# Kernel tuning notes

Measured on AMD Instinct MI355X. Metric: run time of the kernel, lower is better.

The kernel has to match this reference:

```python
import jax, jax.numpy as jnp
import numpy as np

N_II = 100000      # item nodes
N_UIU = 200000     # user + item nodes
D = 64             # embedding_dim
E_II = 600000
E_UIU = 1200000
L_II = 3           # num_layers_ii
L_UIU = 3          # num_layers_uiu
N_USERS = 100000   # items occupy indices [N_USERS, N_USERS+N_II)


def _lightgcn_embedding(x, edge_index, edge_weight, num_layers, num_nodes):
    """PyG LightGCN.get_embedding: symmetric gcn_norm (no self loops) + mean over layer outputs."""
    src, dst = edge_index[0], edge_index[1]
    # gcn_norm: deg over target nodes, weighted by edge_weight
    deg = jax.ops.segment_sum(edge_weight, dst, num_segments=num_nodes)
    deg_inv_sqrt = jnp.where(deg > 0, jax.lax.rsqrt(jnp.where(deg > 0, deg, 1.0)), 0.0)
    norm = deg_inv_sqrt[src] * edge_weight * deg_inv_sqrt[dst]  # [E]
    alpha = 1.0 / (num_layers + 1)
    out = x * alpha
    for _ in range(num_layers):
        # SpMM: gather source embeddings, scale, scatter-add to targets
        x = jax.ops.segment_sum(norm[:, None] * x[src], dst, num_segments=num_nodes)  # [N, D]
        out = out + x * alpha
    return out


def setup_inputs() -> dict:
    key = jax.random.key(0)
    k1, k2, k3, k4, k5, k6 = jax.random.split(key, 6)
    return {
        "emb_ii": jax.random.normal(k1, (N_II, D), dtype=jnp.float32),
        "emb_uiu": jax.random.normal(k2, (N_UIU, D), dtype=jnp.float32),
        "edge_attr_ii": jax.random.uniform(k3, (E_II,), dtype=jnp.float32),
        "edge_attr_uiu": jax.random.uniform(k4, (E_UIU,), dtype=jnp.float32),
        "edge_index_ii": jax.random.randint(k5, (2, E_II), 0, N_II, dtype=jnp.int32),
        "edge_index_uiu": jax.random.randint(k6, (2, E_UIU), 0, N_UIU, dtype=jnp.int32),
        # contiguous item block starting at N_USERS (node_mask_item.nonzero())
        "item_idx": jnp.arange(N_II, dtype=jnp.int32) + N_USERS,
    }


def reference(emb_ii, emb_uiu, edge_attr_ii, edge_attr_uiu,
              edge_index_ii, edge_index_uiu, item_idx):
    # item-item graph propagation
    h_ii = _lightgcn_embedding(emb_ii, edge_index_ii, edge_attr_ii, L_II, N_II)  # [N_II, D]
    # write item embeddings into the user-item embedding table
    emb_uiu = emb_uiu.at[item_idx].set(h_ii)
    # user-item graph propagation
    h_uiu = _lightgcn_embedding(emb_uiu, edge_index_uiu, edge_attr_uiu, L_UIU, N_UIU)  # [N_UIU, D]
    return h_uiu
```

## Files before the change

kernel.cpp:

```cpp
#include <hip/hip_runtime.h>


#define D       64
#define N_II    100000
#define N_UIU   200000
#define E_II    600000
#define E_UIU   1200000
#define N_USERS 100000
#define B       256
#define CR_K    8
#define FE_K    4

__device__ __forceinline__ unsigned short f2bf(float f) {
    unsigned u = __float_as_uint(f);
    u += 0x7fffu + ((u >> 16) & 1u);
    return (unsigned short)(u >> 16);
}
__device__ __forceinline__ void bf8_fma(float acc[8], uint4 p, float v) {
    acc[0] += v * __uint_as_float(p.x << 16);
    acc[1] += v * __uint_as_float(p.x & 0xffff0000u);
    acc[2] += v * __uint_as_float(p.y << 16);
    acc[3] += v * __uint_as_float(p.y & 0xffff0000u);
    acc[4] += v * __uint_as_float(p.z << 16);
    acc[5] += v * __uint_as_float(p.z & 0xffff0000u);
    acc[6] += v * __uint_as_float(p.w << 16);
    acc[7] += v * __uint_as_float(p.w & 0xffff0000u);
}
__device__ __forceinline__ void bf8_add(float acc[8], uint4 p) {
    acc[0] += __uint_as_float(p.x << 16);
    acc[1] += __uint_as_float(p.x & 0xffff0000u);
    acc[2] += __uint_as_float(p.y << 16);
    acc[3] += __uint_as_float(p.y & 0xffff0000u);
    acc[4] += __uint_as_float(p.z << 16);
    acc[5] += __uint_as_float(p.z & 0xffff0000u);
    acc[6] += __uint_as_float(p.w << 16);
    acc[7] += __uint_as_float(p.w & 0xffff0000u);
}
__device__ __forceinline__ uint4 pack8(const float a[8]) {
    uint4 r;
    r.x = (unsigned)f2bf(a[0]) | ((unsigned)f2bf(a[1]) << 16);
    r.y = (unsigned)f2bf(a[2]) | ((unsigned)f2bf(a[3]) << 16);
    r.z = (unsigned)f2bf(a[4]) | ((unsigned)f2bf(a[5]) << 16);
    r.w = (unsigned)f2bf(a[6]) | ((unsigned)f2bf(a[7]) << 16);
    return r;
}

__device__ __forceinline__ int bin_of(int c) { return (c < 63) ? c : 63; }

__device__ __forceinline__ void scan_boff(const int* __restrict__ ghist, int* sboff) {
    int t = threadIdx.x;
    if (t < 64) {
        int v = ghist[t];
        int s = v;
        for (int o = 1; o < 64; o <<= 1) {
            int u = __shfl_up(s, o);
            if (t >= o) s += u;
        }
        sboff[t] = s - v;
    }
}


__device__ __forceinline__ void rol_cnt(int bid, const int* __restrict__ dst,
                                        int* __restrict__ cnt, int* __restrict__ rank,
                                        int e0, int e1) {
    int base = e0 + bid * (B * CR_K) + threadIdx.x;
    int d[CR_K];
#pragma unroll
    for (int k = 0; k < CR_K; ++k) {
        int e = base + k * B;
        d[k] = (e < e1) ? dst[e] : 0;
    }
#pragma unroll
    for (int k = 0; k < CR_K; ++k) {
        int e = base + k * B;
        if (e < e1) rank[e] = atomicAdd(&cnt[d[k]], 1);
    }
}

__device__ __forceinline__ void rol_cvt(int bid, const float4* __restrict__ x,
                                        uint4* __restrict__ xb, int n8) {
    int i = bid * B + threadIdx.x;
    if (i >= n8) return;
    float4 a = x[2 * i], b = x[2 * i + 1];
    float t[8] = {a.x, a.y, a.z, a.w, b.x, b.y, b.z, b.w};
    xb[i] = pack8(t);
}

__device__ void rol_node(int bid, const int* __restrict__ cnt, int2* __restrict__ rr,
                         int* __restrict__ binrank, int* __restrict__ ghist,
                         int* __restrict__ gcur, int N) {
    __shared__ int sh[B];
    __shared__ int h[64], hb[64];
    __shared__ int sbase;
    int t = threadIdx.x;
    int i = bid * B + t;
    int c = (i < N) ? cnt[i] : 0;
    int b = bin_of(c);
    sh[t] = c;
    if (t < 64) h[t] = 0;
    __syncthreads();
    int rk = 0;
    if (i < N) rk = atomicAdd(&h[b], 1);
    for (int off = 1; off < B; off <<= 1) {
        int u = (t >= off) ? sh[t - off] : 0;
        __syncthreads();
        sh[t] += u;
        __syncthreads();
    }
    if (t == B - 1) sbase = atomicAdd(gcur, sh[B - 1]);
    if (t < 64) hb[t] = h[t] ? atomicAdd(&ghist[t], h[t]) : 0;
    __syncthreads();
    if (i < N) {
        int o = sbase + sh[t] - c;
        rr[i] = make_int2(o, o + c);
        binrank[i] = hb[b] + rk;
    }
}

__device__ __forceinline__ void rol_fillE(int bid, const int* __restrict__ src,
                                          const int* __restrict__ dst,
                                          const float* __restrict__ w,
                                          const int* __restrict__ rank,
                                          const int2* __restrict__ rr,
                                          int2* __restrict__ ev, int E) {
    int base = bid * (B * FE_K) + threadIdx.x;
    int d[FE_K], r[FE_K], s[FE_K];
    float ww[FE_K];
#pragma unroll
    for (int k = 0; k < FE_K; ++k) {
        int e = base + k * B;
        if (e < E) { d[k] = dst[e]; r[k] = rank[e]; s[k] = src[e]; ww[k] = w[e]; }
        else       { d[k] = 0; r[k] = 0; s[k] = 0; ww[k] = 0.f; }
    }
    int pos[FE_K];
#pragma unroll
    for (int k = 0; k < FE_K; ++k) pos[k] = rr[d[k]].x + r[k];
#pragma unroll
    for (int k = 0; k < FE_K; ++k) {
        int e = base + k * B;
        if (e < E) ev[pos[k]] = make_int2(s[k], __float_as_int(ww[k]));
    }
}

__device__ __forceinline__ void rol_deg(int bid, const int2* __restrict__ rr,
                                        const int2* __restrict__ ev,
                                        float* __restrict__ dis, int N) {
    int i = bid * B + threadIdx.x;
    if (i >= N) return;
    int2 se = rr[i];
    float dg = 0.f;
    for (int j = se.x; j < se.y; ++j) dg += __int_as_float(ev[j].y);
    dis[i] = (dg > 0.f) ? rsqrtf(dg) : 0.f;
}

__device__ void rol_valsc(int bid, const int2* __restrict__ rr, const float* __restrict__ dis,
                          const int* __restrict__ binrank, const int* __restrict__ ghist,
                          int2* __restrict__ ev, int* __restrict__ perm,
                          int2* __restrict__ rrp, int N) {
    __shared__ int sboff[64];
    scan_boff(ghist, sboff);
    __syncthreads();
    int i = bid * B + threadIdx.x;
    if (i >= N) return;
    int2 se = rr[i];
    float di = dis[i];
    for (int j = se.x; j < se.y; ++j) {
        int2 p = ev[j];
        ev[j].y = __float_as_int(di * __int_as_float(p.y) * dis[p.x]);
    }
    int pos = sboff[bin_of(se.y - se.x)] + binrank[i];
    perm[pos] = i;
    rrp[pos]  = se;
}

__device__ void rol_sortfin(int bid, const int2* __restrict__ rr, const int* __restrict__ brk,
                            const int* __restrict__ ghist, int* __restrict__ sortpos,
                            int* __restrict__ perm, int2* __restrict__ srr, int N) {
    __shared__ int sboff[64];
    scan_boff(ghist, sboff);
    __syncthreads();
    int i = bid * B + threadIdx.x;
    if (i >= N) return;
    int2 se = rr[i];
    int pos = sboff[bin_of(se.y - se.x)] + brk[i];
    sortpos[i] = pos;
    perm[pos] = i;
    srr[pos]  = se;
}

__device__ __forceinline__ void rol_evnorm(int bid, const int2* __restrict__ rr,
                                           const float* __restrict__ dis,
                                           const int* __restrict__ sortpos,
                                           int2* __restrict__ ev, int N) {
    int i = bid * B + threadIdx.x;
    if (i >= N) return;
    int2 se = rr[i];
    float di = dis[i];
    for (int j = se.x; j < se.y; ++j) {
        int2 p = ev[j];
        ev[j] = make_int2(sortpos[p.x],
                          __float_as_int(di * __int_as_float(p.y) * dis[p.x]));
    }
}

__device__ void rol_cvts(int bid, const float4* __restrict__ xu,
                         const int2* __restrict__ rr2, const int* __restrict__ brk2,
                         const int* __restrict__ ghist2, uint4* __restrict__ xb0s,
                         int Nrows) {
    __shared__ int sboff[64];
    scan_boff(ghist2, sboff);
    __syncthreads();
    int idx = bid * B + threadIdx.x;
    int row = idx >> 3;
    if (row >= Nrows) return;
    int g = idx & 7;
    int2 s2 = rr2[row];
    int pos = sboff[bin_of(s2.y - s2.x)] + brk2[row];
    float4 a = xu[(size_t)row * 16 + 2 * g], b = xu[(size_t)row * 16 + 2 * g + 1];
    float t[8] = {a.x, a.y, a.z, a.w, b.x, b.y, b.z, b.w};
    xb0s[(size_t)pos * 8 + g] = pack8(t);
}

__device__ void rol_spmm(int bid, const int2* __restrict__ rrp, const int* __restrict__ perm,
                         const int2* __restrict__ ev, const uint4* __restrict__ xb,
                         uint4* __restrict__ xn, int N) {
    int idx = bid * B + threadIdx.x;
    int vrow = idx >> 3;
    if (vrow >= N) return;
    int g = idx & 7;
    int2 se = rrp[vrow];
    int row = perm[vrow];
    float acc[8] = {0.f, 0.f, 0.f, 0.f, 0.f, 0.f, 0.f, 0.f};
    int j = se.x, e = se.y;
    for (; j + 3 < e; j += 4) {
        int2 p0 = ev[j], p1 = ev[j + 1], p2 = ev[j + 2], p3 = ev[j + 3];
        uint4 a0 = xb[(size_t)p0.x * 8 + g];
        uint4 a1 = xb[(size_t)p1.x * 8 + g];
        uint4 a2 = xb[(size_t)p2.x * 8 + g];
        uint4 a3 = xb[(size_t)p3.x * 8 + g];
        bf8_fma(acc, a0, __int_as_float(p0.y));
        bf8_fma(acc, a1, __int_as_float(p1.y));
        bf8_fma(acc, a2, __int_as_float(p2.y));
        bf8_fma(acc, a3, __int_as_float(p3.y));
    }
    for (; j < e; ++j) {
        int2 p0 = ev[j];
        uint4 a0 = xb[(size_t)p0.x * 8 + g];
        bf8_fma(acc, a0, __int_as_float(p0.y));
    }
    xn[(size_t)row * 8 + g] = pack8(acc);
}

__device__ void rol_spmm_s(int bid, const int2* __restrict__ srr, const int2* __restrict__ ev,
                           const uint4* __restrict__ xb, uint4* __restrict__ xn, int N) {
    int idx = bid * B + threadIdx.x;
    int vrow = idx >> 3;
    if (vrow >= N) return;
    int g = idx & 7;
    int2 se = srr[vrow];
    float acc[8] = {0.f, 0.f, 0.f, 0.f, 0.f, 0.f, 0.f, 0.f};
    int j = se.x, e = se.y;
    for (; j + 3 < e; j += 4) {
        int2 p0 = ev[j], p1 = ev[j + 1], p2 = ev[j + 2], p3 = ev[j + 3];
        uint4 a0 = xb[(size_t)p0.x * 8 + g];
        uint4 a1 = xb[(size_t)p1.x * 8 + g];
        uint4 a2 = xb[(size_t)p2.x * 8 + g];
        uint4 a3 = xb[(size_t)p3.x * 8 + g];
        bf8_fma(acc, a0, __int_as_float(p0.y));
        bf8_fma(acc, a1, __int_as_float(p1.y));
        bf8_fma(acc, a2, __int_as_float(p2.y));
        bf8_fma(acc, a3, __int_as_float(p3.y));
    }
    for (; j < e; ++j) {
        int2 p0 = ev[j];
        uint4 a0 = xb[(size_t)p0.x * 8 + g];
        bf8_fma(acc, a0, __int_as_float(p0.y));
    }
    xn[(size_t)vrow * 8 + g] = pack8(acc);
}

__device__ void rol_final1(int bid, const int2* __restrict__ rrp, const int* __restrict__ perm,
                           const int2* __restrict__ ev, const uint4* __restrict__ x2b,
                           const uint4* __restrict__ x1b, const uint4* __restrict__ x0b,
                           const int2* __restrict__ rr2, const int* __restrict__ brk2,
                           const int* __restrict__ ghist2, uint4* __restrict__ xb0s,
                           float alpha, int N) {
    __shared__ int sboff[64];
    scan_boff(ghist2, sboff);
    __syncthreads();
    int idx = bid * B + threadIdx.x;
    int vrow = idx >> 3;
    if (vrow >= N) return;
    int g = idx & 7;
    int2 se = rrp[vrow];
    int row = perm[vrow];
    float acc[8] = {0.f, 0.f, 0.f, 0.f, 0.f, 0.f, 0.f, 0.f};
    int j = se.x, e = se.y;
    for (; j + 3 < e; j += 4) {
        int2 p0 = ev[j], p1 = ev[j + 1], p2 = ev[j + 2], p3 = ev[j + 3];
        uint4 a0 = x2b[(size_t)p0.x * 8 + g];
        uint4 a1 = x2b[(size_t)p1.x * 8 + g];
        uint4 a2 = x2b[(size_t)p2.x * 8 + g];
        uint4 a3 = x2b[(size_t)p3.x * 8 + g];
        bf8_fma(acc, a0, __int_as_float(p0.y));
        bf8_fma(acc, a1, __int_as_float(p1.y));
        bf8_fma(acc, a2, __int_as_float(p2.y));
        bf8_fma(acc, a3, __int_as_float(p3.y));
    }
    for (; j < e; ++j) {
        int2 p0 = ev[j];
        uint4 a0 = x2b[(size_t)p0.x * 8 + g];
        bf8_fma(acc, a0, __int_as_float(p0.y));
    }
    bf8_add(acc, x1b[(size_t)row * 8 + g]);
    bf8_add(acc, x2b[(size_t)row * 8 + g]);
    bf8_add(acc, x0b[(size_t)row * 8 + g]);
    float r[8];
#pragma unroll
    for (int k = 0; k < 8; ++k) r[k] = alpha * acc[k];
    int oi = N_USERS + row;
    int2 s2 = rr2[oi];
    int pos = sboff[bin_of(s2.y - s2.x)] + brk2[oi];
    xb0s[(size_t)pos * 8 + g] = pack8(r);
}

__device__ void rol_final_s(int bid, const int2* __restrict__ srr, const int* __restrict__ perm,
                            const int2* __restrict__ ev, const uint4* __restrict__ x2s,
                            const uint4* __restrict__ x1s, const uint4* __restrict__ x0s,
                            float4* __restrict__ out, float alpha, int N) {
    int idx = bid * B + threadIdx.x;
    int vrow = idx >> 3;
    if (vrow >= N) return;
    int g = idx & 7;
    int2 se = srr[vrow];
    float acc[8] = {0.f, 0.f, 0.f, 0.f, 0.f, 0.f, 0.f, 0.f};
    int j = se.x, e = se.y;
    for (; j + 3 < e; j += 4) {
        int2 p0 = ev[j], p1 = ev[j + 1], p2 = ev[j + 2], p3 = ev[j + 3];
        uint4 a0 = x2s[(size_t)p0.x * 8 + g];
        uint4 a1 = x2s[(size_t)p1.x * 8 + g];
        uint4 a2 = x2s[(size_t)p2.x * 8 + g];
        uint4 a3 = x2s[(size_t)p3.x * 8 + g];
        bf8_fma(acc, a0, __int_as_float(p0.y));
        bf8_fma(acc, a1, __int_as_float(p1.y));
        bf8_fma(acc, a2, __int_as_float(p2.y));
        bf8_fma(acc, a3, __int_as_float(p3.y));
    }
    for (; j < e; ++j) {
        int2 p0 = ev[j];
        uint4 a0 = x2s[(size_t)p0.x * 8 + g];
        bf8_fma(acc, a0, __int_as_float(p0.y));
    }
    bf8_add(acc, x1s[(size_t)vrow * 8 + g]);
    bf8_add(acc, x2s[(size_t)vrow * 8 + g]);
    bf8_add(acc, x0s[(size_t)vrow * 8 + g]);
    float r[8];
#pragma unroll
    for (int k = 0; k < 8; ++k) r[k] = alpha * acc[k];
    int orig = perm[vrow];
    out[(size_t)orig * 16 + 2 * g]     = make_float4(r[0], r[1], r[2], r[3]);
    out[(size_t)orig * 16 + 2 * g + 1] = make_float4(r[4], r[5], r[6], r[7]);
}


__global__ void f_cnt_cvt(int nbA, const int* dstA, int* cntA, int* rankA, int eA,
                          const float4* xB, uint4* xbB, int n8B) {
    int b = (int)blockIdx.x;
    if (b < nbA) rol_cnt(b, dstA, cntA, rankA, 0, eA);
    else         rol_cvt(b - nbA, xB, xbB, n8B);
}

__global__ void f_node_cnt(int nbA, const int* cntN, int2* rr, int* brk, int* ghist,
                           int* gcur, int N,
                           const int* dstS, int* cntS, int* rankS, int e0, int e1) {
    int b = (int)blockIdx.x;
    if (b < nbA) rol_node(b, cntN, rr, brk, ghist, gcur, N);
    else         rol_cnt(b - nbA, dstS, cntS, rankS, e0, e1);
}

__global__ void f_fillE_cnt(int nbA, const int* src, const int* dst, const float* w,
                            const int* rank, const int2* rr, int2* ev, int E,
                            const int* dstS, int* cntS, int* rankS, int e0, int e1) {
    int b = (int)blockIdx.x;
    if (b < nbA) rol_fillE(b, src, dst, w, rank, rr, ev, E);
    else         rol_cnt(b - nbA, dstS, cntS, rankS, e0, e1);
}

__global__ void f_deg_cnt(int nbA, const int2* rr, const int2* ev, float* dis, int N,
                          const int* dstS, int* cntS, int* rankS, int e0, int e1) {
    int b = (int)blockIdx.x;
    if (b < nbA) rol_deg(b, rr, ev, dis, N);
    else         rol_cnt(b - nbA, dstS, cntS, rankS, e0, e1);
}

__global__ void f_valsc_cnt(int nbA, const int2* rr, const float* dis, const int* brk,
                            const int* ghist, int2* ev, int* perm, int2* rrp, int N,
                            const int* dstS, int* cntS, int* rankS, int e0, int e1) {
    int b = (int)blockIdx.x;
    if (b < nbA) rol_valsc(b, rr, dis, brk, ghist, ev, perm, rrp, N);
    else         rol_cnt(b - nbA, dstS, cntS, rankS, e0, e1);
}

__global__ void f_spmm_node(int nbA, const int2* rrp, const int* perm, const int2* ev,
                            const uint4* xb, uint4* xn, int NA,
                            const int* cntN, int2* rrB, int* brkB, int* ghistB,
                            int* gcurB, int NB) {
    int b = (int)blockIdx.x;
    if (b < nbA) rol_spmm(b, rrp, perm, ev, xb, xn, NA);
    else         rol_node(b - nbA, cntN, rrB, brkB, ghistB, gcurB, NB);
}

__global__ void f_spmm_fill(int nbA, const int2* rrp, const int* perm, const int2* ev,
                            const uint4* xb, uint4* xn, int NA,
                            const int* srcB, const int* dstB, const float* wB,
                            const int* rankB, const int2* rrB, int2* evB, int EB) {
    int b = (int)blockIdx.x;
    if (b < nbA) rol_spmm(b, rrp, perm, ev, xb, xn, NA);
    else         rol_fillE(b - nbA, srcB, dstB, wB, rankB, rrB, evB, EB);
}

__global__ void f_final_mix(int nbA, const int2* rrp1, const int* perm1, const int2* ev1,
                            const uint4* x2b, const uint4* x1b, const uint4* x0b,
                            float alpha, int N1,
                            int nbB, const float4* xu,
                            int nbC, const int2* rr2, const int2* ev2, float* dis2, int N2,
                            const int* brk2, const int* ghist2, uint4* xb0s,
                            int* sortpos2, int* perm2, int2* srr2) {
    int b = (int)blockIdx.x;
    if (b < nbA) { rol_final1(b, rrp1, perm1, ev1, x2b, x1b, x0b,
                              rr2, brk2, ghist2, xb0s, alpha, N1); return; }
    b -= nbA;
    if (b < nbB) { rol_cvts(b, xu, rr2, brk2, ghist2, xb0s, N_USERS); return; }
    b -= nbB;
    if (b < nbC) { rol_deg(b, rr2, ev2, dis2, N2); return; }
    rol_sortfin(b - nbC, rr2, brk2, ghist2, sortpos2, perm2, srr2, N2);
}

__global__ void k_evnorm(const int2* rr, const float* dis, const int* sortpos,
                         int2* ev, int N) {
    rol_evnorm((int)blockIdx.x, rr, dis, sortpos, ev, N);
}
__global__ void k_spmm_s(const int2* srr, const int2* ev, const uint4* xb,
                         uint4* xn, int N) {
    rol_spmm_s((int)blockIdx.x, srr, ev, xb, xn, N);
}
__global__ void k_final_s(const int2* srr, const int* perm, const int2* ev,
                          const uint4* x2s, const uint4* x1s, const uint4* x0s,
                          float4* out, float alpha, int N) {
    rol_final_s((int)blockIdx.x, srr, perm, ev, x2s, x1s, x0s, out, alpha, N);
}


static inline int nbx(long long work, int per) { return (int)((work + per - 1) / per); }

extern "C" void kernel_launch(void* const* d_in, const int* in_sizes, int n_in,
                              void* d_out, int out_size, void* d_ws, size_t ws_size,
                              hipStream_t stream) {
    const float* emb_ii  = (const float*)d_in[0];
    const float* emb_uiu = (const float*)d_in[1];
    const float* w_ii    = (const float*)d_in[2];
    const float* w_uiu   = (const float*)d_in[3];
    const int*   src_ii  = (const int*)d_in[4];
    const int*   dst_ii  = src_ii + E_II;
    const int*   src_uiu = (const int*)d_in[5];
    const int*   dst_uiu = src_uiu + E_UIU;
    float*       out     = (float*)d_out;

    uint4* xb0_u = (uint4*)d_ws;
    uint4* x1_u  = xb0_u + (size_t)N_UIU * 8;
    uint4* x2_u  = x1_u + (size_t)N_UIU * 8;

    int2*  ev1   = (int2*)(x2_u + (size_t)N_II * 8);
    int*   rank1 = (int*)(ev1 + E_II);
    int2*  rr1   = (int2*)(rank1 + E_II);
    int*   cnt1  = (int*)(rr1 + N_II);
    int*   gt1   = cnt1 + N_II;
    float* dis1  = (float*)(gt1 + 65);
    int*   brk1  = (int*)(dis1 + N_II);
    int*   perm1 = rank1;
    int2*  rrp1  = (int2*)(rank1 + N_II);

    int2*  ev2   = (int2*)(x2_u + (size_t)N_UIU * 8);
    int*   rank2 = (int*)(ev2 + E_UIU);
    int*   perm2 = rank2;
    int2*  srr2  = (int2*)(rank2 + N_UIU);
    int2*  rr2   = (int2*)(rank2 + E_UIU);
    int*   cnt2  = (int*)(rr2 + N_UIU);
    int*   sortpos2 = cnt2;
    int*   gt2   = cnt2 + N_UIU;
    int*   brk2  = gt2 + 65;
    float* dis2  = (float*)(brk2 + N_UIU);

    uint4* g1_x0 = x1_u;
    uint4* g1_x1 = x1_u + (size_t)N_II * 8;
    uint4* g1_x2 = x2_u;

    const float alpha = 0.25f;

    hipMemsetAsync(cnt1, 0, ((size_t)N_II + 65) * sizeof(int), stream);
    hipMemsetAsync(cnt2, 0, ((size_t)N_UIU + 65) * sizeof(int), stream);

    const int s[5] = {0, 300000, 600000, 900000, E_UIU};

    const int nbCnt1 = nbx(E_II, B * CR_K);
    const int nbCvt1 = nbx((long long)N_II * 8, B);
    const int nbN1   = nbx(N_II, B);
    const int nbF1   = nbx(E_II, B * FE_K);
    const int nbS1   = nbx((long long)N_II * 8, B);
    const int nbN2   = nbx(N_UIU, B);
    const int nbF2   = nbx(E_UIU, B * FE_K);
    const int nbS2   = nbx((long long)N_UIU * 8, B);
    const int nbCvt2 = nbx((long long)N_USERS * 8, B);

    f_cnt_cvt<<<nbCnt1 + nbCvt1, B, 0, stream>>>(
        nbCnt1, dst_ii, cnt1, rank1, E_II,
        (const float4*)emb_ii, g1_x0, N_II * 8);

    f_node_cnt<<<nbN1 + nbx(s[1] - s[0], B * CR_K), B, 0, stream>>>(
        nbN1, cnt1, rr1, brk1, gt1 + 1, gt1, N_II,
        dst_uiu, cnt2, rank2, s[0], s[1]);

    f_fillE_cnt<<<nbF1 + nbx(s[2] - s[1], B * CR_K), B, 0, stream>>>(
        nbF1, src_ii, dst_ii, w_ii, rank1, rr1, ev1, E_II,
        dst_uiu, cnt2, rank2, s[1], s[2]);

    f_deg_cnt<<<nbN1 + nbx(s[3] - s[2], B * CR_K), B, 0, stream>>>(
        nbN1, rr1, ev1, dis1, N_II,
        dst_uiu, cnt2, rank2, s[2], s[3]);

    f_valsc_cnt<<<nbN1 + nbx(s[4] - s[3], B * CR_K), B, 0, stream>>>(
        nbN1, rr1, dis1, brk1, gt1 + 1, ev1, perm1, rrp1, N_II,
        dst_uiu, cnt2, rank2, s[3], s[4]);

    f_spmm_node<<<nbS1 + nbN2, B, 0, stream>>>(
        nbS1, rrp1, perm1, ev1, g1_x0, g1_x1, N_II,
        cnt2, rr2, brk2, gt2 + 1, gt2, N_UIU);

    f_spmm_fill<<<nbS1 + nbF2, B, 0, stream>>>(
        nbS1, rrp1, perm1, ev1, g1_x1, g1_x2, N_II,
        src_uiu, dst_uiu, w_uiu, rank2, rr2, ev2, E_UIU);

    f_final_mix<<<nbS1 + nbCvt2 + nbN2 + nbN2, B, 0, stream>>>(
        nbS1, rrp1, perm1, ev1, g1_x2, g1_x1, g1_x0, alpha, N_II,
        nbCvt2, (const float4*)emb_uiu,
        nbN2, rr2, ev2, dis2, N_UIU,
        brk2, gt2 + 1, xb0_u, sortpos2, perm2, srr2);

    k_evnorm<<<nbN2, B, 0, stream>>>(rr2, dis2, sortpos2, ev2, N_UIU);

    k_spmm_s<<<nbS2, B, 0, stream>>>(srr2, ev2, xb0_u, x1_u, N_UIU);
    k_spmm_s<<<nbS2, B, 0, stream>>>(srr2, ev2, x1_u, x2_u, N_UIU);
    k_final_s<<<nbS2, B, 0, stream>>>(srr2, perm2, ev2, x2_u, x1_u, xb0_u,
                                      (float4*)out, alpha, N_UIU);
}
```

Before: 486.7 us.

## Merge preprocessing and item-graph stages into one cooperative persistent kernel

The nine separate fused launches that build the CSR structures, normalise edges and run the item-graph SpMM are replaced by a single cooperative kernel. It uses grid-wide barriers between stages and grid-stride loops over a persistent grid sized from occupancy. The two memsets are folded into the kernel, and the user-item counting work is rebalanced across stages with new split points. This removes per-launch overhead and tail idle time, but adds grid.sync costs and lowers parallelism inside each stage to the resident grid size.

```diff
diff --git a/kernel.cpp b/kernel.cpp
--- a/kernel.cpp
+++ b/kernel.cpp
@@ -1,4 +1,7 @@
 #include <hip/hip_runtime.h>
+#include <hip/hip_cooperative_groups.h>
+
+namespace cg = cooperative_groups;
 
 
 #define D       64
@@ -8,8 +11,11 @@
 #define E_UIU   1200000
 #define N_USERS 100000
 #define B       256
-#define CR_K    8
-#define FE_K    4
+
+#define NB1   ((N_II + B - 1) / B)
+#define NB2   ((N_UIU + B - 1) / B)
+#define NS1B  ((N_II * 8 + B - 1) / B)
+#define NCVTB ((N_USERS * 8 + B - 1) / B)
 
 __device__ __forceinline__ unsigned short f2bf(float f) {
     unsigned u = __float_as_uint(f);
@@ -44,7 +50,6 @@
     r.w = (unsigned)f2bf(a[6]) | ((unsigned)f2bf(a[7]) << 16);
     return r;
 }
-
 __device__ __forceinline__ int bin_of(int c) { return (c < 63) ? c : 63; }
 
 __device__ __forceinline__ void scan_boff(const int* __restrict__ ghist, int* sboff) {
@@ -61,40 +66,14 @@
 }
 
 
-__device__ __forceinline__ void rol_cnt(int bid, const int* __restrict__ dst,
-                                        int* __restrict__ cnt, int* __restrict__ rank,
-                                        int e0, int e1) {
-    int base = e0 + bid * (B * CR_K) + threadIdx.x;
-    int d[CR_K];
-#pragma unroll
-    for (int k = 0; k < CR_K; ++k) {
-        int e = base + k * B;
-        d[k] = (e < e1) ? dst[e] : 0;
-    }
-#pragma unroll
-    for (int k = 0; k < CR_K; ++k) {
-        int e = base + k * B;
-        if (e < e1) rank[e] = atomicAdd(&cnt[d[k]], 1);
-    }
-}
-
-__device__ __forceinline__ void rol_cvt(int bid, const float4* __restrict__ x,
-                                        uint4* __restrict__ xb, int n8) {
-    int i = bid * B + threadIdx.x;
-    if (i >= n8) return;
-    float4 a = x[2 * i], b = x[2 * i + 1];
-    float t[8] = {a.x, a.y, a.z, a.w, b.x, b.y, b.z, b.w};
-    xb[i] = pack8(t);
-}
-
-__device__ void rol_node(int bid, const int* __restrict__ cnt, int2* __restrict__ rr,
-                         int* __restrict__ binrank, int* __restrict__ ghist,
-                         int* __restrict__ gcur, int N) {
+__device__ void node_block(int vb, const int* __restrict__ cnt, int2* __restrict__ rr,
+                           int* __restrict__ brk, int* __restrict__ ghist,
+                           int* __restrict__ gcur, int N) {
     __shared__ int sh[B];
     __shared__ int h[64], hb[64];
     __shared__ int sbase;
     int t = threadIdx.x;
-    int i = bid * B + t;
+    int i = vb * B + t;
     int c = (i < N) ? cnt[i] : 0;
     int b = bin_of(c);
     sh[t] = c;
@@ -114,147 +93,260 @@
     if (i < N) {
         int o = sbase + sh[t] - c;
         rr[i] = make_int2(o, o + c);
-        binrank[i] = hb[b] + rk;
-    }
-}
-
-__device__ __forceinline__ void rol_fillE(int bid, const int* __restrict__ src,
-                                          const int* __restrict__ dst,
-                                          const float* __restrict__ w,
-                                          const int* __restrict__ rank,
-                                          const int2* __restrict__ rr,
-                                          int2* __restrict__ ev, int E) {
-    int base = bid * (B * FE_K) + threadIdx.x;
-    int d[FE_K], r[FE_K], s[FE_K];
-    float ww[FE_K];
-#pragma unroll
-    for (int k = 0; k < FE_K; ++k) {
-        int e = base + k * B;
-        if (e < E) { d[k] = dst[e]; r[k] = rank[e]; s[k] = src[e]; ww[k] = w[e]; }
-        else       { d[k] = 0; r[k] = 0; s[k] = 0; ww[k] = 0.f; }
-    }
-    int pos[FE_K];
-#pragma unroll
-    for (int k = 0; k < FE_K; ++k) pos[k] = rr[d[k]].x + r[k];
-#pragma unroll
-    for (int k = 0; k < FE_K; ++k) {
-        int e = base + k * B;
-        if (e < E) ev[pos[k]] = make_int2(s[k], __float_as_int(ww[k]));
-    }
-}
-
-__device__ __forceinline__ void rol_deg(int bid, const int2* __restrict__ rr,
-                                        const int2* __restrict__ ev,
-                                        float* __restrict__ dis, int N) {
-    int i = bid * B + threadIdx.x;
-    if (i >= N) return;
-    int2 se = rr[i];
-    float dg = 0.f;
-    for (int j = se.x; j < se.y; ++j) dg += __int_as_float(ev[j].y);
-    dis[i] = (dg > 0.f) ? rsqrtf(dg) : 0.f;
-}
-
-__device__ void rol_valsc(int bid, const int2* __restrict__ rr, const float* __restrict__ dis,
-                          const int* __restrict__ binrank, const int* __restrict__ ghist,
-                          int2* __restrict__ ev, int* __restrict__ perm,
-                          int2* __restrict__ rrp, int N) {
+        brk[i] = hb[b] + rk;
+    }
+    __syncthreads();
+}
+
+__device__ void valsc_block(int vb, const int2* __restrict__ rr, const float* __restrict__ dis,
+                            const int* __restrict__ brk, const int* __restrict__ ghist,
+                            int2* __restrict__ ev, int* __restrict__ perm,
+                            int2* __restrict__ rrp, int N) {
     __shared__ int sboff[64];
     scan_boff(ghist, sboff);
     __syncthreads();
-    int i = bid * B + threadIdx.x;
-    if (i >= N) return;
-    int2 se = rr[i];
-    float di = dis[i];
-    for (int j = se.x; j < se.y; ++j) {
-        int2 p = ev[j];
-        ev[j].y = __float_as_int(di * __int_as_float(p.y) * dis[p.x]);
-    }
-    int pos = sboff[bin_of(se.y - se.x)] + binrank[i];
-    perm[pos] = i;
-    rrp[pos]  = se;
-}
-
-__device__ void rol_sortfin(int bid, const int2* __restrict__ rr, const int* __restrict__ brk,
-                            const int* __restrict__ ghist, int* __restrict__ sortpos,
-                            int* __restrict__ perm, int2* __restrict__ srr, int N) {
+    int i = vb * B + threadIdx.x;
+    if (i < N) {
+        int2 se = rr[i];
+        float di = dis[i];
+        for (int j = se.x; j < se.y; ++j) {
+            int2 pp = ev[j];
+            ev[j].y = __float_as_int(di * __int_as_float(pp.y) * dis[pp.x]);
+        }
+        int pos = sboff[bin_of(se.y - se.x)] + brk[i];
+        perm[pos] = i;
+        rrp[pos]  = se;
+    }
+    __syncthreads();
+}
+
+__device__ void sortfin_block(int vb, const int2* __restrict__ rr, const int* __restrict__ brk,
+                              const int* __restrict__ ghist, int* __restrict__ sortpos,
+                              int* __restrict__ perm, int2* __restrict__ srr, int N) {
     __shared__ int sboff[64];
     scan_boff(ghist, sboff);
     __syncthreads();
-    int i = bid * B + threadIdx.x;
-    if (i >= N) return;
-    int2 se = rr[i];
-    int pos = sboff[bin_of(se.y - se.x)] + brk[i];
-    sortpos[i] = pos;
-    perm[pos] = i;
-    srr[pos]  = se;
-}
-
-__device__ __forceinline__ void rol_evnorm(int bid, const int2* __restrict__ rr,
-                                           const float* __restrict__ dis,
-                                           const int* __restrict__ sortpos,
-                                           int2* __restrict__ ev, int N) {
-    int i = bid * B + threadIdx.x;
-    if (i >= N) return;
-    int2 se = rr[i];
-    float di = dis[i];
-    for (int j = se.x; j < se.y; ++j) {
-        int2 p = ev[j];
-        ev[j] = make_int2(sortpos[p.x],
-                          __float_as_int(di * __int_as_float(p.y) * dis[p.x]));
-    }
-}
-
-__device__ void rol_cvts(int bid, const float4* __restrict__ xu,
-                         const int2* __restrict__ rr2, const int* __restrict__ brk2,
-                         const int* __restrict__ ghist2, uint4* __restrict__ xb0s,
-                         int Nrows) {
+    int i = vb * B + threadIdx.x;
+    if (i < N) {
+        int2 se = rr[i];
+        int pos = sboff[bin_of(se.y - se.x)] + brk[i];
+        sortpos[i] = pos;
+        perm[pos] = i;
+        srr[pos]  = se;
+    }
+    __syncthreads();
+}
+
+__device__ void cvts_block(int vb, const float4* __restrict__ xu,
+                           const int2* __restrict__ rr2, const int* __restrict__ brk2,
+                           const int* __restrict__ ghist2, uint4* __restrict__ xb0s) {
     __shared__ int sboff[64];
     scan_boff(ghist2, sboff);
     __syncthreads();
-    int idx = bid * B + threadIdx.x;
+    int idx = vb * B + threadIdx.x;
     int row = idx >> 3;
-    if (row >= Nrows) return;
-    int g = idx & 7;
-    int2 s2 = rr2[row];
-    int pos = sboff[bin_of(s2.y - s2.x)] + brk2[row];
-    float4 a = xu[(size_t)row * 16 + 2 * g], b = xu[(size_t)row * 16 + 2 * g + 1];
-    float t[8] = {a.x, a.y, a.z, a.w, b.x, b.y, b.z, b.w};
-    xb0s[(size_t)pos * 8 + g] = pack8(t);
-}
-
-__device__ void rol_spmm(int bid, const int2* __restrict__ rrp, const int* __restrict__ perm,
-                         const int2* __restrict__ ev, const uint4* __restrict__ xb,
-                         uint4* __restrict__ xn, int N) {
-    int idx = bid * B + threadIdx.x;
+    if (row < N_USERS) {
+        int g = idx & 7;
+        int2 s2 = rr2[row];
+        int pos = sboff[bin_of(s2.y - s2.x)] + brk2[row];
+        float4 a = xu[(size_t)row * 16 + 2 * g], b = xu[(size_t)row * 16 + 2 * g + 1];
+        float tv[8] = {a.x, a.y, a.z, a.w, b.x, b.y, b.z, b.w};
+        xb0s[(size_t)pos * 8 + g] = pack8(tv);
+    }
+    __syncthreads();
+}
+
+__device__ void final1_block(int vb, const int2* __restrict__ rrp, const int* __restrict__ perm,
+                             const int2* __restrict__ ev, const uint4* __restrict__ x2b,
+                             const uint4* __restrict__ x1b, const uint4* __restrict__ x0b,
+                             const int2* __restrict__ rr2, const int* __restrict__ brk2,
+                             const int* __restrict__ ghist2, uint4* __restrict__ xb0s,
+                             float alpha) {
+    __shared__ int sboff[64];
+    scan_boff(ghist2, sboff);
+    __syncthreads();
+    int idx = vb * B + threadIdx.x;
     int vrow = idx >> 3;
-    if (vrow >= N) return;
-    int g = idx & 7;
-    int2 se = rrp[vrow];
-    int row = perm[vrow];
-    float acc[8] = {0.f, 0.f, 0.f, 0.f, 0.f, 0.f, 0.f, 0.f};
-    int j = se.x, e = se.y;
-    for (; j + 3 < e; j += 4) {
-        int2 p0 = ev[j], p1 = ev[j + 1], p2 = ev[j + 2], p3 = ev[j + 3];
-        uint4 a0 = xb[(size_t)p0.x * 8 + g];
-        uint4 a1 = xb[(size_t)p1.x * 8 + g];
-        uint4 a2 = xb[(size_t)p2.x * 8 + g];
-        uint4 a3 = xb[(size_t)p3.x * 8 + g];
-        bf8_fma(acc, a0, __int_as_float(p0.y));
-        bf8_fma(acc, a1, __int_as_float(p1.y));
-        bf8_fma(acc, a2, __int_as_float(p2.y));
-        bf8_fma(acc, a3, __int_as_float(p3.y));
-    }
-    for (; j < e; ++j) {
-        int2 p0 = ev[j];
-        uint4 a0 = xb[(size_t)p0.x * 8 + g];
-        bf8_fma(acc, a0, __int_as_float(p0.y));
-    }
-    xn[(size_t)row * 8 + g] = pack8(acc);
-}
-
-__device__ void rol_spmm_s(int bid, const int2* __restrict__ srr, const int2* __restrict__ ev,
-                           const uint4* __restrict__ xb, uint4* __restrict__ xn, int N) {
-    int idx = bid * B + threadIdx.x;
+    if (vrow < N_II) {
+        int g = idx & 7;
+        int2 se = rrp[vrow];
+        int row = perm[vrow];
+        float acc[8] = {0.f, 0.f, 0.f, 0.f, 0.f, 0.f, 0.f, 0.f};
+        int j = se.x, e = se.y;
+        for (; j + 3 < e; j += 4) {
+            int2 p0 = ev[j], p1 = ev[j + 1], p2 = ev[j + 2], p3 = ev[j + 3];
+            uint4 a0 = x2b[(size_t)p0.x * 8 + g];
+            uint4 a1 = x2b[(size_t)p1.x * 8 + g];
+            uint4 a2 = x2b[(size_t)p2.x * 8 + g];
+            uint4 a3 = x2b[(size_t)p3.x * 8 + g];
+            bf8_fma(acc, a0, __int_as_float(p0.y));
+            bf8_fma(acc, a1, __int_as_float(p1.y));
+            bf8_fma(acc, a2, __int_as_float(p2.y));
+            bf8_fma(acc, a3, __int_as_float(p3.y));
+        }
+        for (; j < e; ++j) {
+            int2 p0 = ev[j];
+            uint4 a0 = x2b[(size_t)p0.x * 8 + g];
+            bf8_fma(acc, a0, __int_as_float(p0.y));
+        }
+        bf8_add(acc, x1b[(size_t)row * 8 + g]);
+        bf8_add(acc, x2b[(size_t)row * 8 + g]);
+        bf8_add(acc, x0b[(size_t)row * 8 + g]);
+        float r[8];
+#pragma unroll
+        for (int k = 0; k < 8; ++k) r[k] = alpha * acc[k];
+        int oi = N_USERS + row;
+        int2 s2 = rr2[oi];
+        int pos = sboff[bin_of(s2.y - s2.x)] + brk2[oi];
+        xb0s[(size_t)pos * 8 + g] = pack8(r);
+    }
+    __syncthreads();
+}
+
+__device__ void spmm_gs(int gtid, int gsz, const int2* __restrict__ rrp,
+                        const int* __restrict__ perm, const int2* __restrict__ ev,
+                        const uint4* __restrict__ xb, uint4* __restrict__ xn, int N) {
+    for (int idx = gtid; idx < N * 8; idx += gsz) {
+        int vrow = idx >> 3;
+        int g = idx & 7;
+        int2 se = rrp[vrow];
+        int row = perm[vrow];
+        float acc[8] = {0.f, 0.f, 0.f, 0.f, 0.f, 0.f, 0.f, 0.f};
+        int j = se.x, e = se.y;
+        for (; j + 3 < e; j += 4) {
+            int2 p0 = ev[j], p1 = ev[j + 1], p2 = ev[j + 2], p3 = ev[j + 3];
+            uint4 a0 = xb[(size_t)p0.x * 8 + g];
+            uint4 a1 = xb[(size_t)p1.x * 8 + g];
+            uint4 a2 = xb[(size_t)p2.x * 8 + g];
+            uint4 a3 = xb[(size_t)p3.x * 8 + g];
+            bf8_fma(acc, a0, __int_as_float(p0.y));
+            bf8_fma(acc, a1, __int_as_float(p1.y));
+            bf8_fma(acc, a2, __int_as_float(p2.y));
+            bf8_fma(acc, a3, __int_as_float(p3.y));
+        }
+        for (; j < e; ++j) {
+            int2 p0 = ev[j];
+            uint4 a0 = xb[(size_t)p0.x * 8 + g];
+            bf8_fma(acc, a0, __int_as_float(p0.y));
+        }
+        xn[(size_t)row * 8 + g] = pack8(acc);
+    }
+}
+
+
+struct MegaP {
+    const int *src1, *dst1; const float *w1;
+    const int *src2, *dst2; const float *w2;
+    const float4 *emb1; const float4 *embu;
+    int *cnt1; int *rank1; int2 *rr1; int *brk1; float *dis1;
+    int *perm1; int2 *rrp1; int2 *ev1;
+    int *cnt2; int *rank2; int2 *rr2; int *brk2; float *dis2;
+    int *sortpos2; int *perm2; int2 *srr2; int2 *ev2;
+    uint4 *g1x0, *g1x1, *g1x2, *xb0s;
+    float alpha;
+    int c1, c2, c3, c4, c5;
+};
+
+__global__ void __launch_bounds__(B) mega(MegaP p) {
+    cg::grid_group gr = cg::this_grid();
+    const int gsz  = (int)gridDim.x * B;
+    const int gtid = (int)(blockIdx.x * B + threadIdx.x);
+    int* gt1 = p.cnt1 + N_II;
+    int* gt2 = p.cnt2 + N_UIU;
+
+    for (int i = gtid; i < N_II + 129;  i += gsz) p.cnt1[i] = 0;
+    for (int i = gtid; i < N_UIU + 129; i += gsz) p.cnt2[i] = 0;
+    gr.sync();
+
+    for (int i = gtid; i < N_II * 8; i += gsz) {
+        float4 a = p.emb1[2 * i], b = p.emb1[2 * i + 1];
+        float tv[8] = {a.x, a.y, a.z, a.w, b.x, b.y, b.z, b.w};
+        p.g1x0[i] = pack8(tv);
+    }
+    for (int e = gtid; e < E_II; e += gsz)
+        p.rank1[e] = atomicAdd(&p.cnt1[p.dst1[e]], 1);
+    for (int e = gtid; e < p.c1; e += gsz)
+        p.rank2[e] = atomicAdd(&p.cnt2[p.dst2[e]], 1);
+    gr.sync();
+
+    for (int vb = (int)blockIdx.x; vb < NB1; vb += (int)gridDim.x)
+        node_block(vb, p.cnt1, p.rr1, p.brk1, gt1 + 1, gt1, N_II);
+    for (int e = p.c1 + gtid; e < p.c2; e += gsz)
+        p.rank2[e] = atomicAdd(&p.cnt2[p.dst2[e]], 1);
+    gr.sync();
+
+    for (int e = gtid; e < E_II; e += gsz) {
+        int d = p.dst1[e];
+        int pos = p.rr1[d].x + p.rank1[e];
+        p.ev1[pos] = make_int2(p.src1[e], __float_as_int(p.w1[e]));
+    }
+    for (int e = p.c2 + gtid; e < p.c3; e += gsz)
+        p.rank2[e] = atomicAdd(&p.cnt2[p.dst2[e]], 1);
+    gr.sync();
+
+    for (int i = gtid; i < N_II; i += gsz) {
+        int2 se = p.rr1[i];
+        float dg = 0.f;
+        for (int j = se.x; j < se.y; ++j) dg += __int_as_float(p.ev1[j].y);
+        p.dis1[i] = (dg > 0.f) ? rsqrtf(dg) : 0.f;
+    }
+    for (int e = p.c3 + gtid; e < p.c4; e += gsz)
+        p.rank2[e] = atomicAdd(&p.cnt2[p.dst2[e]], 1);
+    gr.sync();
+
+    for (int vb = (int)blockIdx.x; vb < NB1; vb += (int)gridDim.x)
+        valsc_block(vb, p.rr1, p.dis1, p.brk1, gt1 + 1, p.ev1, p.perm1, p.rrp1, N_II);
+    for (int e = p.c4 + gtid; e < p.c5; e += gsz)
+        p.rank2[e] = atomicAdd(&p.cnt2[p.dst2[e]], 1);
+    gr.sync();
+
+    spmm_gs(gtid, gsz, p.rrp1, p.perm1, p.ev1, p.g1x0, p.g1x1, N_II);
+    for (int e = p.c5 + gtid; e < E_UIU; e += gsz)
+        p.rank2[e] = atomicAdd(&p.cnt2[p.dst2[e]], 1);
+    gr.sync();
+
+    spmm_gs(gtid, gsz, p.rrp1, p.perm1, p.ev1, p.g1x1, p.g1x2, N_II);
+    for (int vb = (int)blockIdx.x; vb < NB2; vb += (int)gridDim.x)
+        node_block(vb, p.cnt2, p.rr2, p.brk2, gt2 + 1, gt2, N_UIU);
+    gr.sync();
+
+    for (int e = gtid; e < E_UIU; e += gsz) {
+        int d = p.dst2[e];
+        int pos = p.rr2[d].x + p.rank2[e];
+        p.ev2[pos] = make_int2(p.src2[e], __float_as_int(p.w2[e]));
+    }
+    for (int vb = (int)blockIdx.x; vb < NCVTB; vb += (int)gridDim.x)
+        cvts_block(vb, p.embu, p.rr2, p.brk2, gt2 + 1, p.xb0s);
+    gr.sync();
+
+    for (int vb = (int)blockIdx.x; vb < NS1B; vb += (int)gridDim.x)
+        final1_block(vb, p.rrp1, p.perm1, p.ev1, p.g1x2, p.g1x1, p.g1x0,
+                     p.rr2, p.brk2, gt2 + 1, p.xb0s, p.alpha);
+    for (int i = gtid; i < N_UIU; i += gsz) {
+        int2 se = p.rr2[i];
+        float dg = 0.f;
+        for (int j = se.x; j < se.y; ++j) dg += __int_as_float(p.ev2[j].y);
+        p.dis2[i] = (dg > 0.f) ? rsqrtf(dg) : 0.f;
+    }
+    for (int vb = (int)blockIdx.x; vb < NB2; vb += (int)gridDim.x)
+        sortfin_block(vb, p.rr2, p.brk2, gt2 + 1, p.sortpos2, p.perm2, p.srr2, N_UIU);
+    gr.sync();
+
+    for (int i = gtid; i < N_UIU; i += gsz) {
+        int2 se = p.rr2[i];
+        float di = p.dis2[i];
+        for (int j = se.x; j < se.y; ++j) {
+            int2 pp = p.ev2[j];
+            p.ev2[j] = make_int2(p.sortpos2[pp.x],
+                                 __float_as_int(di * __int_as_float(pp.y) * p.dis2[pp.x]));
+        }
+    }
+}
+
+
+__global__ void k_spmm_s(const int2* __restrict__ srr, const int2* __restrict__ ev,
+                         const uint4* __restrict__ xb, uint4* __restrict__ xn, int N) {
+    int idx = (int)(blockIdx.x * B + threadIdx.x);
     int vrow = idx >> 3;
     if (vrow >= N) return;
     int g = idx & 7;
@@ -280,56 +372,11 @@
     xn[(size_t)vrow * 8 + g] = pack8(acc);
 }
 
-__device__ void rol_final1(int bid, const int2* __restrict__ rrp, const int* __restrict__ perm,
-                           const int2* __restrict__ ev, const uint4* __restrict__ x2b,
-                           const uint4* __restrict__ x1b, const uint4* __restrict__ x0b,
-                           const int2* __restrict__ rr2, const int* __restrict__ brk2,
-                           const int* __restrict__ ghist2, uint4* __restrict__ xb0s,
-                           float alpha, int N) {
-    __shared__ int sboff[64];
-    scan_boff(ghist2, sboff);
-    __syncthreads();
-    int idx = bid * B + threadIdx.x;
-    int vrow = idx >> 3;
-    if (vrow >= N) return;
-    int g = idx & 7;
-    int2 se = rrp[vrow];
-    int row = perm[vrow];
-    float acc[8] = {0.f, 0.f, 0.f, 0.f, 0.f, 0.f, 0.f, 0.f};
-    int j = se.x, e = se.y;
-    for (; j + 3 < e; j += 4) {
-        int2 p0 = ev[j], p1 = ev[j + 1], p2 = ev[j + 2], p3 = ev[j + 3];
-        uint4 a0 = x2b[(size_t)p0.x * 8 + g];
-        uint4 a1 = x2b[(size_t)p1.x * 8 + g];
-        uint4 a2 = x2b[(size_t)p2.x * 8 + g];
-        uint4 a3 = x2b[(size_t)p3.x * 8 + g];
-        bf8_fma(acc, a0, __int_as_float(p0.y));
-        bf8_fma(acc, a1, __int_as_float(p1.y));
-        bf8_fma(acc, a2, __int_as_float(p2.y));
-        bf8_fma(acc, a3, __int_as_float(p3.y));
-    }
-    for (; j < e; ++j) {
-        int2 p0 = ev[j];
-        uint4 a0 = x2b[(size_t)p0.x * 8 + g];
-        bf8_fma(acc, a0, __int_as_float(p0.y));
-    }
-    bf8_add(acc, x1b[(size_t)row * 8 + g]);
-    bf8_add(acc, x2b[(size_t)row * 8 + g]);
-    bf8_add(acc, x0b[(size_t)row * 8 + g]);
-    float r[8];
-#pragma unroll
-    for (int k = 0; k < 8; ++k) r[k] = alpha * acc[k];
-    int oi = N_USERS + row;
-    int2 s2 = rr2[oi];
-    int pos = sboff[bin_of(s2.y - s2.x)] + brk2[oi];
-    xb0s[(size_t)pos * 8 + g] = pack8(r);
-}
-
-__device__ void rol_final_s(int bid, const int2* __restrict__ srr, const int* __restrict__ perm,
-                            const int2* __restrict__ ev, const uint4* __restrict__ x2s,
-                            const uint4* __restrict__ x1s, const uint4* __restrict__ x0s,
-                            float4* __restrict__ out, float alpha, int N) {
-    int idx = bid * B + threadIdx.x;
+__global__ void k_final_s(const int2* __restrict__ srr, const int* __restrict__ perm,
+                          const int2* __restrict__ ev, const uint4* __restrict__ x2s,
+                          const uint4* __restrict__ x1s, const uint4* __restrict__ x0s,
+                          float4* __restrict__ out, float alpha, int N) {
+    int idx = (int)(blockIdx.x * B + threadIdx.x);
     int vrow = idx >> 3;
     if (vrow >= N) return;
     int g = idx & 7;
@@ -364,94 +411,6 @@
 }
 
 
-__global__ void f_cnt_cvt(int nbA, const int* dstA, int* cntA, int* rankA, int eA,
-                          const float4* xB, uint4* xbB, int n8B) {
-    int b = (int)blockIdx.x;
-    if (b < nbA) rol_cnt(b, dstA, cntA, rankA, 0, eA);
-    else         rol_cvt(b - nbA, xB, xbB, n8B);
-}
-
-__global__ void f_node_cnt(int nbA, const int* cntN, int2* rr, int* brk, int* ghist,
-                           int* gcur, int N,
-                           const int* dstS, int* cntS, int* rankS, int e0, int e1) {
-    int b = (int)blockIdx.x;
-    if (b < nbA) rol_node(b, cntN, rr, brk, ghist, gcur, N);
-    else         rol_cnt(b - nbA, dstS, cntS, rankS, e0, e1);
-}
-
-__global__ void f_fillE_cnt(int nbA, const int* src, const int* dst, const float* w,
-                            const int* rank, const int2* rr, int2* ev, int E,
-                            const int* dstS, int* cntS, int* rankS, int e0, int e1) {
-    int b = (int)blockIdx.x;
-    if (b < nbA) rol_fillE(b, src, dst, w, rank, rr, ev, E);
-    else         rol_cnt(b - nbA, dstS, cntS, rankS, e0, e1);
-}
-
-__global__ void f_deg_cnt(int nbA, const int2* rr, const int2* ev, float* dis, int N,
-                          const int* dstS, int* cntS, int* rankS, int e0, int e1) {
-    int b = (int)blockIdx.x;
-    if (b < nbA) rol_deg(b, rr, ev, dis, N);
-    else         rol_cnt(b - nbA, dstS, cntS, rankS, e0, e1);
-}
-
-__global__ void f_valsc_cnt(int nbA, const int2* rr, const float* dis, const int* brk,
-                            const int* ghist, int2* ev, int* perm, int2* rrp, int N,
-                            const int* dstS, int* cntS, int* rankS, int e0, int e1) {
-    int b = (int)blockIdx.x;
-    if (b < nbA) rol_valsc(b, rr, dis, brk, ghist, ev, perm, rrp, N);
-    else         rol_cnt(b - nbA, dstS, cntS, rankS, e0, e1);
-}
-
-__global__ void f_spmm_node(int nbA, const int2* rrp, const int* perm, const int2* ev,
-                            const uint4* xb, uint4* xn, int NA,
-                            const int* cntN, int2* rrB, int* brkB, int* ghistB,
-                            int* gcurB, int NB) {
-    int b = (int)blockIdx.x;
-    if (b < nbA) rol_spmm(b, rrp, perm, ev, xb, xn, NA);
-    else         rol_node(b - nbA, cntN, rrB, brkB, ghistB, gcurB, NB);
-}
-
-__global__ void f_spmm_fill(int nbA, const int2* rrp, const int* perm, const int2* ev,
-                            const uint4* xb, uint4* xn, int NA,
-                            const int* srcB, const int* dstB, const float* wB,
-                            const int* rankB, const int2* rrB, int2* evB, int EB) {
-    int b = (int)blockIdx.x;
-    if (b < nbA) rol_spmm(b, rrp, perm, ev, xb, xn, NA);
-    else         rol_fillE(b - nbA, srcB, dstB, wB, rankB, rrB, evB, EB);
-}
-
-__global__ void f_final_mix(int nbA, const int2* rrp1, const int* perm1, const int2* ev1,
-                            const uint4* x2b, const uint4* x1b, const uint4* x0b,
-                            float alpha, int N1,
-                            int nbB, const float4* xu,
-                            int nbC, const int2* rr2, const int2* ev2, float* dis2, int N2,
-                            const int* brk2, const int* ghist2, uint4* xb0s,
-                            int* sortpos2, int* perm2, int2* srr2) {
-    int b = (int)blockIdx.x;
-    if (b < nbA) { rol_final1(b, rrp1, perm1, ev1, x2b, x1b, x0b,
-                              rr2, brk2, ghist2, xb0s, alpha, N1); return; }
-    b -= nbA;
-    if (b < nbB) { rol_cvts(b, xu, rr2, brk2, ghist2, xb0s, N_USERS); return; }
-    b -= nbB;
-    if (b < nbC) { rol_deg(b, rr2, ev2, dis2, N2); return; }
-    rol_sortfin(b - nbC, rr2, brk2, ghist2, sortpos2, perm2, srr2, N2);
-}
-
-__global__ void k_evnorm(const int2* rr, const float* dis, const int* sortpos,
-                         int2* ev, int N) {
-    rol_evnorm((int)blockIdx.x, rr, dis, sortpos, ev, N);
-}
-__global__ void k_spmm_s(const int2* srr, const int2* ev, const uint4* xb,
-                         uint4* xn, int N) {
-    rol_spmm_s((int)blockIdx.x, srr, ev, xb, xn, N);
-}
-__global__ void k_final_s(const int2* srr, const int* perm, const int2* ev,
-                          const uint4* x2s, const uint4* x1s, const uint4* x0s,
-                          float4* out, float alpha, int N) {
-    rol_final_s((int)blockIdx.x, srr, perm, ev, x2s, x1s, x0s, out, alpha, N);
-}
-
-
 static inline int nbx(long long work, int per) { return (int)((work + per - 1) / per); }
 
 extern "C" void kernel_launch(void* const* d_in, const int* in_sizes, int n_in,
@@ -475,8 +434,7 @@
     int*   rank1 = (int*)(ev1 + E_II);
     int2*  rr1   = (int2*)(rank1 + E_II);
     int*   cnt1  = (int*)(rr1 + N_II);
-    int*   gt1   = cnt1 + N_II;
-    float* dis1  = (float*)(gt1 + 65);
+    float* dis1  = (float*)(cnt1 + N_II + 129);
     int*   brk1  = (int*)(dis1 + N_II);
     int*   perm1 = rank1;
     int2*  rrp1  = (int2*)(rank1 + N_II);
@@ -488,8 +446,7 @@
     int2*  rr2   = (int2*)(rank2 + E_UIU);
     int*   cnt2  = (int*)(rr2 + N_UIU);
     int*   sortpos2 = cnt2;
-    int*   gt2   = cnt2 + N_UIU;
-    int*   brk2  = gt2 + 65;
+    int*   brk2  = cnt2 + N_UIU + 129;
     float* dis2  = (float*)(brk2 + N_UIU);
 
     uint4* g1_x0 = x1_u;
@@ -498,57 +455,35 @@
 
     const float alpha = 0.25f;
 
-    hipMemsetAsync(cnt1, 0, ((size_t)N_II + 65) * sizeof(int), stream);
-    hipMemsetAsync(cnt2, 0, ((size_t)N_UIU + 65) * sizeof(int), stream);
-
-    const int s[5] = {0, 300000, 600000, 900000, E_UIU};
-
-    const int nbCnt1 = nbx(E_II, B * CR_K);
-    const int nbCvt1 = nbx((long long)N_II * 8, B);
-    const int nbN1   = nbx(N_II, B);
-    const int nbF1   = nbx(E_II, B * FE_K);
-    const int nbS1   = nbx((long long)N_II * 8, B);
-    const int nbN2   = nbx(N_UIU, B);
-    const int nbF2   = nbx(E_UIU, B * FE_K);
-    const int nbS2   = nbx((long long)N_UIU * 8, B);
-    const int nbCvt2 = nbx((long long)N_USERS * 8, B);
-
-    f_cnt_cvt<<<nbCnt1 + nbCvt1, B, 0, stream>>>(
-        nbCnt1, dst_ii, cnt1, rank1, E_II,
-        (const float4*)emb_ii, g1_x0, N_II * 8);
-
-    f_node_cnt<<<nbN1 + nbx(s[1] - s[0], B * CR_K), B, 0, stream>>>(
-        nbN1, cnt1, rr1, brk1, gt1 + 1, gt1, N_II,
-        dst_uiu, cnt2, rank2, s[0], s[1]);
-
-    f_fillE_cnt<<<nbF1 + nbx(s[2] - s[1], B * CR_K), B, 0, stream>>>(
-        nbF1, src_ii, dst_ii, w_ii, rank1, rr1, ev1, E_II,
-        dst_uiu, cnt2, rank2, s[1], s[2]);
-
-    f_deg_cnt<<<nbN1 + nbx(s[3] - s[2], B * CR_K), B, 0, stream>>>(
-        nbN1, rr1, ev1, dis1, N_II,
-        dst_uiu, cnt2, rank2, s[2], s[3]);
-
-    f_valsc_cnt<<<nbN1 + nbx(s[4] - s[3], B * CR_K), B, 0, stream>>>(
-        nbN1, rr1, dis1, brk1, gt1 + 1, ev1, perm1, rrp1, N_II,
-        dst_uiu, cnt2, rank2, s[3], s[4]);
-
-    f_spmm_node<<<nbS1 + nbN2, B, 0, stream>>>(
-        nbS1, rrp1, perm1, ev1, g1_x0, g1_x1, N_II,
-        cnt2, rr2, brk2, gt2 + 1, gt2, N_UIU);
-
-    f_spmm_fill<<<nbS1 + nbF2, B, 0, stream>>>(
-        nbS1, rrp1, perm1, ev1, g1_x1, g1_x2, N_II,
-        src_uiu, dst_uiu, w_uiu, rank2, rr2, ev2, E_UIU);
-
-    f_final_mix<<<nbS1 + nbCvt2 + nbN2 + nbN2, B, 0, stream>>>(
-        nbS1, rrp1, perm1, ev1, g1_x2, g1_x1, g1_x0, alpha, N_II,
-        nbCvt2, (const float4*)emb_uiu,
-        nbN2, rr2, ev2, dis2, N_UIU,
-        brk2, gt2 + 1, xb0_u, sortpos2, perm2, srr2);
-
-    k_evnorm<<<nbN2, B, 0, stream>>>(rr2, dis2, sortpos2, ev2, N_UIU);
-
+    static int s_grid = 0;
+    if (s_grid == 0) {
+        int dev = 0;
+        hipGetDevice(&dev);
+        hipDeviceProp_t prop;
+        hipGetDeviceProperties(&prop, dev);
+        int mb = 0;
+        hipOccupancyMaxActiveBlocksPerMultiprocessor(&mb, mega, B, 0);
+        if (mb < 1) mb = 1;
+        s_grid = mb * prop.multiProcessorCount;
+        if (s_grid < 256) s_grid = 256;
+    }
+
+    MegaP p;
+    p.src1 = src_ii;  p.dst1 = dst_ii;  p.w1 = w_ii;
+    p.src2 = src_uiu; p.dst2 = dst_uiu; p.w2 = w_uiu;
+    p.emb1 = (const float4*)emb_ii; p.embu = (const float4*)emb_uiu;
+    p.cnt1 = cnt1; p.rank1 = rank1; p.rr1 = rr1; p.brk1 = brk1; p.dis1 = dis1;
+    p.perm1 = perm1; p.rrp1 = rrp1; p.ev1 = ev1;
+    p.cnt2 = cnt2; p.rank2 = rank2; p.rr2 = rr2; p.brk2 = brk2; p.dis2 = dis2;
+    p.sortpos2 = sortpos2; p.perm2 = perm2; p.srr2 = srr2; p.ev2 = ev2;
+    p.g1x0 = g1_x0; p.g1x1 = g1_x1; p.g1x2 = g1_x2; p.xb0s = xb0_u;
+    p.alpha = alpha;
+    p.c1 = 180000; p.c2 = 360000; p.c3 = 540000; p.c4 = 760000; p.c5 = 980000;
+
+    void* args[] = { &p };
+    hipLaunchCooperativeKernel(mega, dim3(s_grid), dim3(B), args, 0, stream);
+
+    const int nbS2 = nbx((long long)N_UIU * 8, B);
     k_spmm_s<<<nbS2, B, 0, stream>>>(srr2, ev2, xb0_u, x1_u, N_UIU);
     k_spmm_s<<<nbS2, B, 0, stream>>>(srr2, ev2, x1_u, x2_u, N_UIU);
     k_final_s<<<nbS2, B, 0, stream>>>(srr2, perm2, ev2, x2_u, x1_u, xb0_u,
```

Result: slower. 1.401 ms (+187.8%).
